# Kernel tuning notes

Measured on AMD Instinct MI355X. Metric: run time of the kernel, lower is better.

## Reference

```python
import jax, jax.numpy as jnp
import numpy as np

B, N, DIM, HEADS, DIM_HEAD = 1, 8192, 512, 8, 64  # dim == heads*dim_head required by pos_emb
EPS = 1e-12  # F.normalize eps


def setup_inputs() -> dict:
    key = jax.random.key(0)
    ks = jax.random.split(key, 13)
    w = lambda k, shape: jax.random.normal(k, shape, dtype=jnp.float32) * 0.02
    return {
        "x_in": jax.random.normal(ks[0], (B, N, DIM), dtype=jnp.float32),
        "task_x": jax.random.normal(ks[1], (B, N, DIM), dtype=jnp.float32),
        "Ges": jax.random.uniform(ks[2], (1, 1, N, N), dtype=jnp.float32) / N,  # OT transport plan (precomputed constant)
        "Wq": w(ks[3], (DIM, DIM)),
        "Wk": w(ks[4], (DIM, DIM)),
        "Wv": w(ks[5], (DIM, DIM)),
        "rescale": jnp.ones((HEADS, 1, 1), dtype=jnp.float32),
        "Wp": w(ks[6], (DIM, DIM)),
        "bp": jnp.zeros((DIM,), dtype=jnp.float32),
        "W1": w(ks[7], (DIM, DIM)),
        "b1": jnp.zeros((DIM,), dtype=jnp.float32),
        "W2": w(ks[8], (DIM, DIM)),
        "b2": jnp.zeros((DIM,), dtype=jnp.float32),
    }


def _l2norm(x):
    # F.normalize(p=2, dim=-1): x / max(||x||, eps)
    n = jnp.sqrt(jnp.sum(x * x, axis=-1, keepdims=True))
    return x / jnp.maximum(n, EPS)


def reference(x_in, task_x, Ges, Wq, Wk, Wv, rescale, Wp, bp, W1, b1, W2, b2):
    b, n, c = x_in.shape
    q_inp = x_in @ Wq.T          # [b,n,hd]
    k_inp = x_in @ Wk.T
    v_inp = x_in @ Wv.T
    split = lambda t: t.reshape(b, n, HEADS, DIM_HEAD).transpose(0, 2, 1, 3)  # [b,h,n,d]
    q, k, v, tx = split(q_inp), split(k_inp), split(v_inp), split(task_x)
    guided = (Ges @ tx) * v       # [b,h,n,d]: OT-guided embedding multiply
    # channel attention: operate along n, attend over d
    qT = _l2norm(q.transpose(0, 1, 3, 2))   # [b,h,d,n]
    kT = _l2norm(k.transpose(0, 1, 3, 2))   # [b,h,d,n]
    gT = guided.transpose(0, 1, 3, 2)        # [b,h,d,n]
    attn = jnp.einsum('bhdn,bhen->bhde', kT, qT) * rescale  # [b,h,d,d]
    attn = jax.nn.softmax(attn, axis=-1)
    x = attn @ gT                 # [b,h,d,n]
    x = x.transpose(0, 3, 1, 2).reshape(b, n, HEADS * DIM_HEAD)  # [b,n,hd]
    out_c = x @ Wp.T + bp
    out_p = (jax.nn.gelu(v_inp @ W1.T + b1, approximate=False)) @ W2.T + b2
    return out_c + out_p
```

## Files before the change

### kernel.cpp

```cpp
#include <hip/hip_runtime.h>
#include <hip/hip_bf16.h>

typedef unsigned short u16;
typedef __attribute__((ext_vector_type(8))) short short8v;
typedef __attribute__((ext_vector_type(4))) float f32x4;

typedef __attribute__((address_space(3))) char lds_char;
typedef const __attribute__((address_space(1))) char g_char;

__device__ __forceinline__ u16 f2bf(float f) {
    union { float f; unsigned int u; } x; x.f = f;
    unsigned int u = x.u;
    unsigned int r = (u + 0x7FFFu + ((u >> 16) & 1u)) >> 16;
    return (u16)r;
}
__device__ __forceinline__ float bf2f(u16 h) {
    union { unsigned int u; float f; } x; x.u = ((unsigned int)h) << 16;
    return x.f;
}
__device__ __forceinline__ void gload16(const void* g, void* l) {
    __builtin_amdgcn_global_load_lds((g_char*)g, (lds_char*)l, 16, 0, 0);
}

template<int EPI, bool AF32>
__global__ __launch_bounds__(512, (AF32 ? 2 : 4)) void gemm_k(
    const void* __restrict__ Ap, int lda,
    const u16* __restrict__ Bt, int ldb,
    void* __restrict__ Cp, int ldc, int K,
    const float* __restrict__ bias,
    const u16* __restrict__ vmul, int ldv)
{
    constexpr int ATB = AF32 ? 32768 : 16384;
    constexpr int BTB = 16384;
    __shared__ alignas(16) char smem[2 * (ATB + BTB)];

    const int t    = threadIdx.x;
    const int m0   = blockIdx.x * 128;
    const int n0   = blockIdx.y * 128;
    const int lane = t & 63;
    const int wid  = t >> 6;
    const int wr   = wid >> 2;
    const int wc   = wid & 3;
    const int lr   = lane & 15;
    const int q4   = lane >> 4;

    f32x4 acc[4][2];
    #pragma unroll
    for (int i = 0; i < 4; ++i)
        #pragma unroll
        for (int j = 0; j < 2; ++j)
            acc[i][j] = (f32x4){0.f, 0.f, 0.f, 0.f};

    auto stage = [&](int b, int kt) {
        const int k0 = kt << 6;
        char* base = smem + b * (ATB + BTB);
        if constexpr (AF32) {
            const float* A32 = (const float*)Ap;
            #pragma unroll
            for (int r = 0; r < 4; ++r) {
                int o   = r * 8192 + t * 16;
                int row = o >> 8;
                int cb  = (o & 255) ^ ((row & 15) << 4);
                const float* gp = A32 + (size_t)(m0 + row) * (size_t)lda + k0 + (cb >> 2);
                gload16(gp, base + r * 8192 + wid * 1024);
            }
        } else {
            const u16* A16 = (const u16*)Ap;
            #pragma unroll
            for (int r = 0; r < 2; ++r) {
                int o   = r * 8192 + t * 16;
                int row = o >> 7;
                int cb  = (o & 127) ^ ((row & 7) << 4);
                const u16* gp = A16 + (size_t)(m0 + row) * (size_t)lda + k0 + (cb >> 1);
                gload16(gp, base + r * 8192 + wid * 1024);
            }
        }
        char* bb = base + ATB;
        #pragma unroll
        for (int r = 0; r < 2; ++r) {
            int o   = r * 8192 + t * 16;
            int row = o >> 7;
            int cb  = (o & 127) ^ ((row & 7) << 4);
            const u16* gp = Bt + (size_t)(n0 + row) * (size_t)ldb + k0 + (cb >> 1);
            gload16(gp, bb + r * 8192 + wid * 1024);
        }
    };

    auto compute = [&](int b) {
        char* base = smem + b * (ATB + BTB);
        char* bb = base + ATB;
        #pragma unroll
        for (int kh = 0; kh < 2; ++kh) {
            short8v a[4], bf[2];
            #pragma unroll
            for (int mi = 0; mi < 4; ++mi) {
                const int ar = wr * 64 + mi * 16 + lr;
                if constexpr (AF32) {
                    const int cb0 = kh * 128 + q4 * 32;
                    const int c0 = cb0 ^ ((ar & 15) << 4);
                    const int c1 = (cb0 + 16) ^ ((ar & 15) << 4);
                    f32x4 f0 = *(const f32x4*)(base + ar * 256 + c0);
                    f32x4 f1 = *(const f32x4*)(base + ar * 256 + c1);
                    short8v av;
                    #pragma unroll
                    for (int j = 0; j < 4; ++j) {
                        av[j]     = (short)__builtin_bit_cast(u16, __float2bfloat16(f0[j]));
                        av[j + 4] = (short)__builtin_bit_cast(u16, __float2bfloat16(f1[j]));
                    }
                    a[mi] = av;
                } else {
                    const int cb = kh * 64 + q4 * 16;
                    const int cp = cb ^ ((ar & 7) << 4);
                    a[mi] = *(const short8v*)(base + ar * 128 + cp);
                }
            }
            #pragma unroll
            for (int ni = 0; ni < 2; ++ni) {
                const int br = wc * 32 + ni * 16 + lr;
                const int cb = kh * 64 + q4 * 16;
                const int cp = cb ^ ((br & 7) << 4);
                bf[ni] = *(const short8v*)(bb + br * 128 + cp);
            }
            #pragma unroll
            for (int mi = 0; mi < 4; ++mi)
                #pragma unroll
                for (int ni = 0; ni < 2; ++ni)
                    acc[mi][ni] = __builtin_amdgcn_mfma_f32_16x16x32_bf16(
                        a[mi], bf[ni], acc[mi][ni], 0, 0, 0);
        }
    };

    const int nsteps = K >> 6;
    stage(0, 0);
    __syncthreads();
    int cur = 0;
    for (int kt = 0; kt < nsteps; ++kt) {
        if (kt + 1 < nsteps) stage(cur ^ 1, kt + 1);
        compute(cur);
        __syncthreads();
        cur ^= 1;
    }

    #pragma unroll
    for (int mi = 0; mi < 4; ++mi) {
        #pragma unroll
        for (int ni = 0; ni < 2; ++ni) {
            const int gc = n0 + wc * 32 + ni * 16 + lr;
            #pragma unroll
            for (int j = 0; j < 4; ++j) {
                const int gr = m0 + wr * 64 + mi * 16 + q4 * 4 + j;
                float v = acc[mi][ni][j];
                if constexpr (EPI == 0) {
                    ((u16*)Cp)[(size_t)gr * ldc + gc] = f2bf(v);
                } else if constexpr (EPI == 1) {
                    v *= bf2f(vmul[(size_t)gr * ldv + gc]);
                    ((u16*)Cp)[(size_t)gr * ldc + gc] = f2bf(v);
                } else if constexpr (EPI == 2) {
                    float x = v + bias[gc];
                    float g = 0.5f * x * (1.0f + erff(x * 0.70710678118f));
                    ((u16*)Cp)[(size_t)gr * ldc + gc] = f2bf(g);
                } else {
                    ((float*)Cp)[(size_t)gr * ldc + gc] = v + bias[gc];
                }
            }
        }
    }
}

__global__ void k_convert(const float* __restrict__ x_in,
                          const float* __restrict__ Wq, const float* __restrict__ Wk,
                          const float* __restrict__ Wv, const float* __restrict__ W1,
                          u16* __restrict__ XB, u16* __restrict__ WqkvB,
                          u16* __restrict__ W1B)
{
    const int C1 = 1048576;
    const int C2 = 196608;
    const int C3 = 65536;
    for (int i = blockIdx.x * blockDim.x + threadIdx.x; i < C1 + C2 + C3;
         i += gridDim.x * blockDim.x) {
        const float* src; u16* dst;
        if (i < C1) { src = x_in + (size_t)i * 4; dst = XB + (size_t)i * 4; }
        else if (i < C1 + C2) {
            int e = (i - C1) * 4;
            if (e < 262144)      src = Wq + e;
            else if (e < 524288) src = Wk + (e - 262144);
            else                 src = Wv + (e - 524288);
            dst = WqkvB + e;
        } else {
            int e = (i - C1 - C2) * 4;
            src = W1 + e; dst = W1B + e;
        }
        float4 v = *reinterpret_cast<const float4*>(src);
        ushort4 h;
        h.x = f2bf(v.x); h.y = f2bf(v.y); h.z = f2bf(v.z); h.w = f2bf(v.w);
        *reinterpret_cast<ushort4*>(dst) = h;
    }
}

__global__ void k_transpose(const float* __restrict__ tx, u16* __restrict__ txt)
{
    __shared__ float tile[64][65];
    const int n0 = blockIdx.x * 64;
    const int c0 = blockIdx.y * 64;
    const int t = threadIdx.x;
    #pragma unroll
    for (int p = 0; p < 4; ++p) {
        int q = p * 256 + t;
        int r = q >> 4, s = q & 15;
        float4 v = *reinterpret_cast<const float4*>(tx + (size_t)(n0 + r) * 512 + c0 + s * 4);
        tile[r][s * 4 + 0] = v.x; tile[r][s * 4 + 1] = v.y;
        tile[r][s * 4 + 2] = v.z; tile[r][s * 4 + 3] = v.w;
    }
    __syncthreads();
    #pragma unroll
    for (int p = 0; p < 4; ++p) {
        int q = p * 256 + t;
        int cc = q >> 4, s = q & 15;
        ushort4 h;
        h.x = f2bf(tile[s * 4 + 0][cc]); h.y = f2bf(tile[s * 4 + 1][cc]);
        h.z = f2bf(tile[s * 4 + 2][cc]); h.w = f2bf(tile[s * 4 + 3][cc]);
        *reinterpret_cast<ushort4*>(txt + (size_t)(c0 + cc) * 8192 + n0 + s * 4) = h;
    }
}

__global__ void k_colsq(const u16* __restrict__ QKV, float* __restrict__ colsq)
{
    const int t = threadIdx.x;
    const int c8 = t & 127, rs = t >> 7;
    float a[8];
    #pragma unroll
    for (int j = 0; j < 8; ++j) a[j] = 0.f;
    const int row0 = blockIdx.x * 64;
    for (int rr = rs; rr < 64; rr += 2) {
        uint4 u = *reinterpret_cast<const uint4*>(QKV + (size_t)(row0 + rr) * 1536 + c8 * 8);
        unsigned int w[4] = {u.x, u.y, u.z, u.w};
        #pragma unroll
        for (int q = 0; q < 4; ++q) {
            float f0 = bf2f((u16)(w[q] & 0xffffu));
            float f1 = bf2f((u16)(w[q] >> 16));
            a[2 * q]     += f0 * f0;
            a[2 * q + 1] += f1 * f1;
        }
    }
    #pragma unroll
    for (int j = 0; j < 8; ++j) atomicAdd(&colsq[c8 * 8 + j], a[j]);
}

__global__ void k_gram(const u16* __restrict__ QKV, float* __restrict__ Sb)
{
    __shared__ u16 Qt[4][64];
    __shared__ u16 Kt[4][64];
    const int h = blockIdx.x >> 6;
    const int chunk = blockIdx.x & 63;
    const int t = threadIdx.x;
    const int e = t & 63;
    const int dg = t >> 6;
    float acc[16];
    #pragma unroll
    for (int k = 0; k < 16; ++k) acc[k] = 0.f;
    const int rowbase = chunk * 128;
    for (int p = 0; p < 32; ++p) {
        __syncthreads();
        if (t < 64) {
            const int mat = t >> 5, sub = t & 31, r = sub >> 3, seg = sub & 7;
            const int row = rowbase + p * 4 + r;
            const int col = (mat ? 512 : 0) + h * 64 + seg * 8;
            uint4 v = *reinterpret_cast<const uint4*>(QKV + (size_t)row * 1536 + col);
            u16* dst = mat ? &Kt[r][seg * 8] : &Qt[r][seg * 8];
            *reinterpret_cast<uint4*>(dst) = v;
        }
        __syncthreads();
        #pragma unroll
        for (int r = 0; r < 4; ++r) {
            const float q = bf2f(Qt[r][e]);
            short8v kv0 = *reinterpret_cast<const short8v*>(&Kt[r][dg * 16]);
            short8v kv1 = *reinterpret_cast<const short8v*>(&Kt[r][dg * 16 + 8]);
            #pragma unroll
            for (int k = 0; k < 8; ++k) {
                acc[k]     += bf2f((u16)kv0[k]) * q;
                acc[k + 8] += bf2f((u16)kv1[k]) * q;
            }
        }
    }
    #pragma unroll
    for (int k = 0; k < 16; ++k)
        atomicAdd(&Sb[h * 4096 + (dg * 16 + k) * 64 + e], acc[k]);
}

__global__ void k_softmax(const float* __restrict__ Sb, const float* __restrict__ colsq,
                          const float* __restrict__ rescale, float* __restrict__ Abuf)
{
    const int h = blockIdx.x;
    const int t = threadIdx.x;
    const float rsc = rescale[h];
    const float nq = fmaxf(sqrtf(colsq[h * 64 + t]), 1e-12f);
    for (int d = 0; d < 64; ++d) {
        const float nk = fmaxf(sqrtf(colsq[512 + h * 64 + d]), 1e-12f);
        float v = Sb[h * 4096 + d * 64 + t] / (nk * nq) * rsc;
        float m = v;
        #pragma unroll
        for (int off = 32; off > 0; off >>= 1) m = fmaxf(m, __shfl_xor(m, off, 64));
        float p = expf(v - m);
        float s = p;
        #pragma unroll
        for (int off = 32; off > 0; off >>= 1) s += __shfl_xor(s, off, 64);
        Abuf[h * 4096 + d * 64 + t] = p / s;
    }
}

__global__ void k_buildbt(const float* __restrict__ Abuf, const float* __restrict__ Wp,
                          const float* __restrict__ W2, const float* __restrict__ bp,
                          const float* __restrict__ b2, u16* __restrict__ BtC,
                          float* __restrict__ bsum)
{
    const int g = blockIdx.x * 256 + threadIdx.x;
    const int j = g >> 10, c = g & 1023;
    if (c < 512) {
        const int h = c >> 6, e = c & 63;
        const float* Ah = Abuf + h * 4096 + e;
        const float* Wph = Wp + (size_t)j * 512 + h * 64;
        float s = 0.f;
        #pragma unroll 8
        for (int d = 0; d < 64; ++d) s += Ah[d * 64] * Wph[d];
        BtC[(size_t)j * 1024 + c] = f2bf(s);
        if (c == 0) bsum[j] = bp[j] + b2[j];
    } else {
        BtC[(size_t)j * 1024 + c] = f2bf(W2[(size_t)j * 512 + (c - 512)]);
    }
}

extern "C" void kernel_launch(void* const* d_in, const int* in_sizes, int n_in,
                              void* d_out, int out_size, void* d_ws, size_t ws_size,
                              hipStream_t stream)
{
    const float* x_in    = (const float*)d_in[0];
    const float* task_x  = (const float*)d_in[1];
    const float* Ges     = (const float*)d_in[2];
    const float* Wq      = (const float*)d_in[3];
    const float* Wk      = (const float*)d_in[4];
    const float* Wv      = (const float*)d_in[5];
    const float* rescale = (const float*)d_in[6];
    const float* Wp      = (const float*)d_in[7];
    const float* bp      = (const float*)d_in[8];
    const float* W1      = (const float*)d_in[9];
    const float* b1      = (const float*)d_in[10];
    const float* W2      = (const float*)d_in[11];
    const float* b2      = (const float*)d_in[12];
    float* out = (float*)d_out;
    char* ws = (char*)d_ws;

    u16*   XB    = (u16*)  (ws + 0);
    u16*   TXT   = (u16*)  (ws + 8388608);
    u16*   QKV   = (u16*)  (ws + 16777216);
    u16*   AH    = (u16*)  (ws + 41943040);
    u16*   WqkvB = (u16*)  (ws + 58720256);
    u16*   W1B   = (u16*)  (ws + 60293120);
    u16*   BtC   = (u16*)  (ws + 60817408);
    float* colsq = (float*)(ws + 61865984);
    float* Sb    = (float*)(ws + 61870080);
    float* Abuf  = (float*)(ws + 62001152);
    float* bsum  = (float*)(ws + 62132224);
    (void)in_sizes; (void)n_in; (void)out_size; (void)ws_size;

    hipMemsetAsync(colsq, 0, 4096 + 131072, stream);

    k_convert  <<<2048, 256, 0, stream>>>(x_in, Wq, Wk, Wv, W1, XB, WqkvB, W1B);
    k_transpose<<<dim3(128, 8), 256, 0, stream>>>(task_x, TXT);

    gemm_k<0, false><<<dim3(64, 12), 512, 0, stream>>>(
        XB, 512, WqkvB, 512, QKV, 1536, 512, nullptr, nullptr, 0);

    k_colsq  <<<128, 256, 0, stream>>>(QKV, colsq);
    k_gram   <<<512, 256, 0, stream>>>(QKV, Sb);
    k_softmax<<<8, 64, 0, stream>>>(Sb, colsq, rescale, Abuf);
    k_buildbt<<<2048, 256, 0, stream>>>(Abuf, Wp, W2, bp, b2, BtC, bsum);

    gemm_k<1, true><<<dim3(64, 4), 512, 0, stream>>>(
        Ges, 8192, TXT, 8192, AH, 1024, 8192, nullptr, QKV + 1024, 1536);

    gemm_k<2, false><<<dim3(64, 4), 512, 0, stream>>>(
        QKV + 1024, 1536, W1B, 512, AH + 512, 1024, 512, b1, nullptr, 0);

    gemm_k<3, false><<<dim3(64, 4), 512, 0, stream>>>(
        AH, 1024, BtC, 1024, out, 512, 1024, bsum, nullptr, 0);
}
```

Baseline: 371.3 us.

## Deepen GEMM K-loop pipeline with explicit vmcnt waits and raw barriers

Replaces the double-buffered stage/compute loop with a multi-stage ring buffer (three stages for fp32-A GEMMs, two otherwise). It issues several tiles of global-to-LDS loads ahead and uses counted s_waitcnt vmcnt waits, so only the oldest tile is waited on. Raw s_barrier calls wrapped in sched_barrier replace __syncthreads. The aim is to hide global load latency behind MFMA work. The trade-off is more LDS per block for the fp32 variant, which may cut occupancy. The hard-coded load counts per stage must also match what stage() actually issues.

```diff
diff --git a/kernel.cpp b/kernel.cpp
--- a/kernel.cpp
+++ b/kernel.cpp
@@ -20,6 +20,14 @@
 }
 __device__ __forceinline__ void gload16(const void* g, void* l) {
     __builtin_amdgcn_global_load_lds((g_char*)g, (lds_char*)l, 16, 0, 0);
+}
+template<int N> __device__ __forceinline__ void vm_wait() {
+    asm volatile("s_waitcnt vmcnt(%0)" :: "i"(N) : "memory");
+}
+__device__ __forceinline__ void barrier_raw() {
+    __builtin_amdgcn_sched_barrier(0);
+    __builtin_amdgcn_s_barrier();
+    __builtin_amdgcn_sched_barrier(0);
 }
 
 template<int EPI, bool AF32>
@@ -30,9 +38,11 @@
     const float* __restrict__ bias,
     const u16* __restrict__ vmul, int ldv)
 {
-    constexpr int ATB = AF32 ? 32768 : 16384;
-    constexpr int BTB = 16384;
-    __shared__ alignas(16) char smem[2 * (ATB + BTB)];
+    constexpr int ATB   = AF32 ? 32768 : 16384;
+    constexpr int BTB   = 16384;
+    constexpr int DEPTH = AF32 ? 3 : 2;
+    constexpr int LPS   = AF32 ? 6 : 4;
+    __shared__ alignas(16) char smem[DEPTH * (ATB + BTB)];
 
     const int t    = threadIdx.x;
     const int m0   = blockIdx.x * 128;
@@ -131,14 +141,28 @@
     };
 
     const int nsteps = K >> 6;
-    stage(0, 0);
-    __syncthreads();
+    #pragma unroll
+    for (int d = 0; d < DEPTH; ++d) stage(d, d);
+
     int cur = 0;
-    for (int kt = 0; kt < nsteps; ++kt) {
-        if (kt + 1 < nsteps) stage(cur ^ 1, kt + 1);
+    for (int kt = 0; kt + DEPTH < nsteps; ++kt) {
+        vm_wait<LPS * (DEPTH - 1)>();
+        barrier_raw();
         compute(cur);
-        __syncthreads();
+        barrier_raw();
+        stage(cur, kt + DEPTH);
+        cur = (cur + 1 == DEPTH) ? 0 : cur + 1;
+    }
+    if constexpr (DEPTH == 3) {
+        vm_wait<2 * LPS>(); barrier_raw(); compute(cur); barrier_raw();
+        cur = (cur + 1 == DEPTH) ? 0 : cur + 1;
+        vm_wait<LPS>();     barrier_raw(); compute(cur); barrier_raw();
+        cur = (cur + 1 == DEPTH) ? 0 : cur + 1;
+        vm_wait<0>();       barrier_raw(); compute(cur);
+    } else {
+        vm_wait<LPS>(); barrier_raw(); compute(cur); barrier_raw();
         cur ^= 1;
+        vm_wait<0>();   barrier_raw(); compute(cur);
     }
 
     #pragma unroll
```

After: 339.0 us. 1.1x faster.

## Restructure GEMM pipeline with register-staged A conversion and fewer, larger wave tiles

Applied to the files above, without the earlier changes.

Rewrites the GEMM main loop. A is loaded into registers, converted from fp32 to bf16 once, and written into LDS in bf16. B uses a triple-buffered direct global-to-LDS path with explicit vmcnt waits and barriers. Blocks drop to 4 waves, each computing a 64x64 tile, so each MFMA operand load is reused more. The x_in bf16 pre-conversion is removed and the QKV GEMM now reads fp32 directly. This aims to cut per-k-step conversion work and barrier overhead in the dominant Ges GEMM. In exchange it raises register pressure, may lower occupancy, and relies on hand-counted waitcnt values.

```diff
diff --git a/kernel.cpp b/kernel.cpp
--- a/kernel.cpp
+++ b/kernel.cpp
@@ -11,8 +11,7 @@
 __device__ __forceinline__ u16 f2bf(float f) {
     union { float f; unsigned int u; } x; x.f = f;
     unsigned int u = x.u;
-    unsigned int r = (u + 0x7FFFu + ((u >> 16) & 1u)) >> 16;
-    return (u16)r;
+    return (u16)((u + 0x7FFFu + ((u >> 16) & 1u)) >> 16);
 }
 __device__ __forceinline__ float bf2f(u16 h) {
     union { unsigned int u; float f; } x; x.u = ((unsigned int)h) << 16;
@@ -21,131 +20,164 @@
 __device__ __forceinline__ void gload16(const void* g, void* l) {
     __builtin_amdgcn_global_load_lds((g_char*)g, (lds_char*)l, 16, 0, 0);
 }
+template<int N> __device__ __forceinline__ void vm_wait() {
+    asm volatile("s_waitcnt vmcnt(%0)" :: "i"(N) : "memory");
+}
+__device__ __forceinline__ void lgkm_barrier() {
+    __builtin_amdgcn_sched_barrier(0);
+    asm volatile("s_waitcnt lgkmcnt(0)" ::: "memory");
+    __builtin_amdgcn_s_barrier();
+    __builtin_amdgcn_sched_barrier(0);
+}
 
 template<int EPI, bool AF32>
-__global__ __launch_bounds__(512, (AF32 ? 2 : 4)) void gemm_k(
+__global__ __launch_bounds__(256, 2) void gemm_k(
     const void* __restrict__ Ap, int lda,
     const u16* __restrict__ Bt, int ldb,
     void* __restrict__ Cp, int ldc, int K,
     const float* __restrict__ bias,
     const u16* __restrict__ vmul, int ldv)
 {
-    constexpr int ATB = AF32 ? 32768 : 16384;
-    constexpr int BTB = 16384;
-    __shared__ alignas(16) char smem[2 * (ATB + BTB)];
+    __shared__ alignas(16) char smem[81920];
+    constexpr int AR  = AF32 ? 8 : 4;
+    constexpr int LPS = AF32 ? 12 : 8;
 
     const int t    = threadIdx.x;
+    const int lane = t & 63;
+    const int wid  = t >> 6;
     const int m0   = blockIdx.x * 128;
     const int n0   = blockIdx.y * 128;
-    const int lane = t & 63;
-    const int wid  = t >> 6;
-    const int wr   = wid >> 2;
-    const int wc   = wid & 3;
-    const int lr   = lane & 15;
-    const int q4   = lane >> 4;
-
-    f32x4 acc[4][2];
+    const int wr   = wid >> 1, wc = wid & 1;
+    const int lr   = lane & 15, q4 = lane >> 4;
+
+    f32x4 acc[4][4];
     #pragma unroll
     for (int i = 0; i < 4; ++i)
         #pragma unroll
-        for (int j = 0; j < 2; ++j)
+        for (int j = 0; j < 4; ++j)
             acc[i][j] = (f32x4){0.f, 0.f, 0.f, 0.f};
 
-    auto stage = [&](int b, int kt) {
+    uint4 rA0[AR], rA1[AR];
+    const int nsteps = K >> 6;
+
+    auto loadA = [&](uint4* r, int kt) {
         const int k0 = kt << 6;
-        char* base = smem + b * (ATB + BTB);
         if constexpr (AF32) {
             const float* A32 = (const float*)Ap;
             #pragma unroll
-            for (int r = 0; r < 4; ++r) {
-                int o   = r * 8192 + t * 16;
-                int row = o >> 8;
-                int cb  = (o & 255) ^ ((row & 15) << 4);
-                const float* gp = A32 + (size_t)(m0 + row) * (size_t)lda + k0 + (cb >> 2);
-                gload16(gp, base + r * 8192 + wid * 1024);
+            for (int p = 0; p < 8; ++p) {
+                int row = wid * 32 + p * 4 + (lane >> 4);
+                r[p] = *(const uint4*)(A32 + (size_t)(m0 + row) * (size_t)lda
+                                       + k0 + (lane & 15) * 4);
             }
         } else {
             const u16* A16 = (const u16*)Ap;
             #pragma unroll
-            for (int r = 0; r < 2; ++r) {
-                int o   = r * 8192 + t * 16;
-                int row = o >> 7;
-                int cb  = (o & 127) ^ ((row & 7) << 4);
-                const u16* gp = A16 + (size_t)(m0 + row) * (size_t)lda + k0 + (cb >> 1);
-                gload16(gp, base + r * 8192 + wid * 1024);
-            }
-        }
-        char* bb = base + ATB;
-        #pragma unroll
-        for (int r = 0; r < 2; ++r) {
-            int o   = r * 8192 + t * 16;
+            for (int p = 0; p < 4; ++p) {
+                int row = wid * 32 + p * 8 + (lane >> 3);
+                r[p] = *(const uint4*)(A16 + (size_t)(m0 + row) * (size_t)lda
+                                       + k0 + (lane & 7) * 8);
+            }
+        }
+    };
+    auto stageB = [&](int boff, int kt) {
+        const int k0 = kt << 6;
+        #pragma unroll
+        for (int p = 0; p < 4; ++p) {
+            int o   = p * 4096 + t * 16;
             int row = o >> 7;
             int cb  = (o & 127) ^ ((row & 7) << 4);
-            const u16* gp = Bt + (size_t)(n0 + row) * (size_t)ldb + k0 + (cb >> 1);
-            gload16(gp, bb + r * 8192 + wid * 1024);
+            gload16(Bt + (size_t)(n0 + row) * (size_t)ldb + k0 + (cb >> 1),
+                    smem + 32768 + boff + o);
         }
     };
-
-    auto compute = [&](int b) {
-        char* base = smem + b * (ATB + BTB);
-        char* bb = base + ATB;
+    auto writeA = [&](const uint4* r, int aoff) {
+        char* base = smem + aoff;
+        if constexpr (AF32) {
+            #pragma unroll
+            for (int p = 0; p < 8; ++p) {
+                int row = wid * 32 + p * 4 + (lane >> 4);
+                int gq  = lane & 15;
+                const float* f = (const float*)&r[p];
+                uint2 w;
+                w.x = (unsigned)f2bf(f[0]) | ((unsigned)f2bf(f[1]) << 16);
+                w.y = (unsigned)f2bf(f[2]) | ((unsigned)f2bf(f[3]) << 16);
+                int sw = (((gq >> 1) * 16) ^ ((row & 7) << 4)) | ((gq & 1) * 8);
+                *(uint2*)(base + row * 128 + sw) = w;
+            }
+        } else {
+            #pragma unroll
+            for (int p = 0; p < 4; ++p) {
+                int row = wid * 32 + p * 8 + (lane >> 3);
+                int gq  = lane & 7;
+                int sw = (gq * 16) ^ ((row & 7) << 4);
+                *(uint4*)(base + row * 128 + sw) = r[p];
+            }
+        }
+    };
+    auto compute = [&](int aoff, int boff) {
+        const char* Ab = smem + aoff;
+        const char* Bb = smem + 32768 + boff;
         #pragma unroll
         for (int kh = 0; kh < 2; ++kh) {
-            short8v a[4], bf[2];
-            #pragma unroll
-            for (int mi = 0; mi < 4; ++mi) {
-                const int ar = wr * 64 + mi * 16 + lr;
-                if constexpr (AF32) {
-                    const int cb0 = kh * 128 + q4 * 32;
-                    const int c0 = cb0 ^ ((ar & 15) << 4);
-                    const int c1 = (cb0 + 16) ^ ((ar & 15) << 4);
-                    f32x4 f0 = *(const f32x4*)(base + ar * 256 + c0);
-                    f32x4 f1 = *(const f32x4*)(base + ar * 256 + c1);
-                    short8v av;
-                    #pragma unroll
-                    for (int j = 0; j < 4; ++j) {
-                        av[j]     = (short)__builtin_bit_cast(u16, __float2bfloat16(f0[j]));
-                        av[j + 4] = (short)__builtin_bit_cast(u16, __float2bfloat16(f1[j]));
-                    }
-                    a[mi] = av;
-                } else {
-                    const int cb = kh * 64 + q4 * 16;
-                    const int cp = cb ^ ((ar & 7) << 4);
-                    a[mi] = *(const short8v*)(base + ar * 128 + cp);
-                }
-            }
-            #pragma unroll
-            for (int ni = 0; ni < 2; ++ni) {
-                const int br = wc * 32 + ni * 16 + lr;
-                const int cb = kh * 64 + q4 * 16;
-                const int cp = cb ^ ((br & 7) << 4);
-                bf[ni] = *(const short8v*)(bb + br * 128 + cp);
+            short8v a[4], b[4];
+            #pragma unroll
+            for (int i = 0; i < 4; ++i) {
+                int ar = wr * 64 + i * 16 + lr;
+                a[i] = *(const short8v*)(Ab + ar * 128 +
+                        ((kh * 64 + q4 * 16) ^ ((ar & 7) << 4)));
+            }
+            #pragma unroll
+            for (int i = 0; i < 4; ++i) {
+                int br = wc * 64 + i * 16 + lr;
+                b[i] = *(const short8v*)(Bb + br * 128 +
+                        ((kh * 64 + q4 * 16) ^ ((br & 7) << 4)));
             }
             #pragma unroll
             for (int mi = 0; mi < 4; ++mi)
                 #pragma unroll
-                for (int ni = 0; ni < 2; ++ni)
+                for (int ni = 0; ni < 4; ++ni)
                     acc[mi][ni] = __builtin_amdgcn_mfma_f32_16x16x32_bf16(
-                        a[mi], bf[ni], acc[mi][ni], 0, 0, 0);
+                        a[mi], b[ni], acc[mi][ni], 0, 0, 0);
         }
     };
-
-    const int nsteps = K >> 6;
-    stage(0, 0);
-    __syncthreads();
-    int cur = 0;
-    for (int kt = 0; kt < nsteps; ++kt) {
-        if (kt + 1 < nsteps) stage(cur ^ 1, kt + 1);
-        compute(cur);
-        __syncthreads();
-        cur ^= 1;
-    }
+    auto rot = [](int x) { return x == 32768 ? 0 : x + 16384; };
+
+    stageB(0, 0);      loadA(rA0, 0);
+    stageB(16384, 1);  loadA(rA1, 1);
+    vm_wait<LPS>();
+    writeA(rA0, 0);
+    lgkm_barrier();
+
+    int brd = 0;
+    int bwr = 32768;
+
+    for (int kt = 0; kt < nsteps - 3; kt += 2) {
+        stageB(bwr, kt + 2); loadA(rA0, kt + 2);
+        vm_wait<LPS>();
+        writeA(rA1, 16384);
+        compute(0, brd);
+        lgkm_barrier();
+        brd = rot(brd); bwr = rot(bwr);
+        stageB(bwr, kt + 3); loadA(rA1, kt + 3);
+        vm_wait<LPS>();
+        writeA(rA0, 0);
+        compute(16384, brd);
+        lgkm_barrier();
+        brd = rot(brd); bwr = rot(bwr);
+    }
+    vm_wait<0>();
+    writeA(rA1, 16384);
+    compute(0, brd);
+    lgkm_barrier();
+    brd = rot(brd);
+    compute(16384, brd);
 
     #pragma unroll
     for (int mi = 0; mi < 4; ++mi) {
         #pragma unroll
-        for (int ni = 0; ni < 2; ++ni) {
-            const int gc = n0 + wc * 32 + ni * 16 + lr;
+        for (int ni = 0; ni < 4; ++ni) {
+            const int gc = n0 + wc * 64 + ni * 16 + lr;
             #pragma unroll
             for (int j = 0; j < 4; ++j) {
                 const int gr = m0 + wr * 64 + mi * 16 + q4 * 4 + j;
@@ -167,27 +199,23 @@
     }
 }
 
-__global__ void k_convert(const float* __restrict__ x_in,
-                          const float* __restrict__ Wq, const float* __restrict__ Wk,
+__global__ void k_convert(const float* __restrict__ Wq, const float* __restrict__ Wk,
                           const float* __restrict__ Wv, const float* __restrict__ W1,
-                          u16* __restrict__ XB, u16* __restrict__ WqkvB,
-                          u16* __restrict__ W1B)
-{
-    const int C1 = 1048576;
+                          u16* __restrict__ WqkvB, u16* __restrict__ W1B)
+{
     const int C2 = 196608;
     const int C3 = 65536;
-    for (int i = blockIdx.x * blockDim.x + threadIdx.x; i < C1 + C2 + C3;
+    for (int i = blockIdx.x * blockDim.x + threadIdx.x; i < C2 + C3;
          i += gridDim.x * blockDim.x) {
         const float* src; u16* dst;
-        if (i < C1) { src = x_in + (size_t)i * 4; dst = XB + (size_t)i * 4; }
-        else if (i < C1 + C2) {
-            int e = (i - C1) * 4;
+        if (i < C2) {
+            int e = i * 4;
             if (e < 262144)      src = Wq + e;
             else if (e < 524288) src = Wk + (e - 262144);
             else                 src = Wv + (e - 524288);
             dst = WqkvB + e;
         } else {
-            int e = (i - C1 - C2) * 4;
+            int e = (i - C2) * 4;
             src = W1 + e; dst = W1B + e;
         }
         float4 v = *reinterpret_cast<const float4*>(src);
@@ -349,7 +377,6 @@
     float* out = (float*)d_out;
     char* ws = (char*)d_ws;
 
-    u16*   XB    = (u16*)  (ws + 0);
     u16*   TXT   = (u16*)  (ws + 8388608);
     u16*   QKV   = (u16*)  (ws + 16777216);
     u16*   AH    = (u16*)  (ws + 41943040);
@@ -364,23 +391,23 @@
 
     hipMemsetAsync(colsq, 0, 4096 + 131072, stream);
 
-    k_convert  <<<2048, 256, 0, stream>>>(x_in, Wq, Wk, Wv, W1, XB, WqkvB, W1B);
+    k_convert  <<<1024, 256, 0, stream>>>(Wq, Wk, Wv, W1, WqkvB, W1B);
     k_transpose<<<dim3(128, 8), 256, 0, stream>>>(task_x, TXT);
 
-    gemm_k<0, false><<<dim3(64, 12), 512, 0, stream>>>(
-        XB, 512, WqkvB, 512, QKV, 1536, 512, nullptr, nullptr, 0);
+    gemm_k<0, true><<<dim3(64, 12), 256, 0, stream>>>(
+        x_in, 512, WqkvB, 512, QKV, 1536, 512, nullptr, nullptr, 0);
 
     k_colsq  <<<128, 256, 0, stream>>>(QKV, colsq);
     k_gram   <<<512, 256, 0, stream>>>(QKV, Sb);
     k_softmax<<<8, 64, 0, stream>>>(Sb, colsq, rescale, Abuf);
     k_buildbt<<<2048, 256, 0, stream>>>(Abuf, Wp, W2, bp, b2, BtC, bsum);
 
-    gemm_k<1, true><<<dim3(64, 4), 512, 0, stream>>>(
+    gemm_k<1, true><<<dim3(64, 4), 256, 0, stream>>>(
         Ges, 8192, TXT, 8192, AH, 1024, 8192, nullptr, QKV + 1024, 1536);
 
-    gemm_k<2, false><<<dim3(64, 4), 512, 0, stream>>>(
+    gemm_k<2, false><<<dim3(64, 4), 256, 0, stream>>>(
         QKV + 1024, 1536, W1B, 512, AH + 512, 1024, 512, b1, nullptr, 0);
 
-    gemm_k<3, false><<<dim3(64, 4), 512, 0, stream>>>(
+    gemm_k<3, false><<<dim3(64, 4), 256, 0, stream>>>(
         AH, 1024, BtC, 1024, out, 512, 1024, bsum, nullptr, 0);
 }
```

Result: slower. 439.5 us (+18.4%).
